# Kernel tuning notes

Measured on AMD Instinct MI355X. Metric: run time of the kernel, lower is better.

## Reference

```python
import jax, jax.numpy as jnp
import numpy as np

D_MODEL, N_HEADS, HEAD_DIM, D_STATE, CHUNK, N_GROUPS = 3584, 112, 64, 64, 256, 2


def setup_inputs() -> dict:
    key = jax.random.key(0)
    ks = jax.random.split(key, 8)
    b, l = 1, 4096
    inner = N_HEADS * HEAD_DIM
    scale = 0.02  # keep activations well-scaled (nn.Linear-ish init)
    return {
        "hidden_states": jax.random.normal(ks[0], (b, l, D_MODEL), jnp.float32),
        "W_in": jax.random.normal(ks[1], (2 * inner, D_MODEL), jnp.float32) * scale,
        "W_out": jax.random.normal(ks[2], (D_MODEL, inner), jnp.float32) * scale,
        "A_log": jax.random.normal(ks[3], (N_HEADS,), jnp.float32),
        "D": jnp.ones((N_HEADS,), jnp.float32),
        "dt_bias": jax.random.normal(ks[4], (N_HEADS,), jnp.float32),
        "B": jax.random.normal(ks[5], (b, l, N_GROUPS, D_STATE), jnp.float32),
        "C": jax.random.normal(ks[6], (b, l, N_GROUPS, D_STATE), jnp.float32),
    }


def _segsum(x):
    # x: [..., T] -> [..., T, T]; segsum[i,j] = sum_{j<k<=i} x[k], -inf above diag
    T = x.shape[-1]
    cs = jnp.cumsum(x, axis=-1)
    diff = cs[..., :, None] - cs[..., None, :]
    mask = jnp.tril(jnp.ones((T, T), bool))
    return jnp.where(mask, diff, -jnp.inf)


def reference(hidden_states, W_in, W_out, A_log, D, dt_bias, B, C):
    b, l, _ = hidden_states.shape
    h, p, n, c = N_HEADS, HEAD_DIM, D_STATE, CHUNK
    nc = l // c

    xz = hidden_states @ W_in.T                       # [b,l,2*h*p]
    x, z = jnp.split(xz, 2, axis=-1)
    x = x.reshape(b, l, h, p)

    dt = jnp.full((b, l, h), 0.1, hidden_states.dtype)  # module uses constant 0.1
    A = -jnp.exp(A_log)                                  # [h]
    dt_sp = jax.nn.softplus(dt + dt_bias)                # [b,l,h]

    # expand group-shared B/C to per-head
    Bh = jnp.repeat(B, h // N_GROUPS, axis=2)            # [b,l,h,n]
    Ch = jnp.repeat(C, h // N_GROUPS, axis=2)

    xdt = x * dt_sp[..., None]                           # discretized input dt*x

    # chunked views: k = chunk index, i/j = position within chunk
    xc = xdt.reshape(b, nc, c, h, p)
    Bc = Bh.reshape(b, nc, c, h, n)
    Cc = Ch.reshape(b, nc, c, h, n)
    dA = (dt_sp * A).reshape(b, nc, c, h).transpose(0, 3, 1, 2)  # [b,h,nc,c]
    dA_cs = jnp.cumsum(dA, axis=-1)                               # [b,h,nc,c]

    # 1) intra-chunk (diagonal blocks)
    L = jnp.exp(_segsum(dA))                                      # [b,h,nc,c,c]
    Y_diag = jnp.einsum('bkihn,bkjhn,bhkij,bkjhp->bkihp', Cc, Bc, L, xc)

    # 2) per-chunk end states
    decay_states = jnp.exp(dA_cs[..., -1:] - dA_cs)               # [b,h,nc,c]
    states = jnp.einsum('bkjhn,bhkj,bkjhp->bkhpn', Bc, decay_states, xc)

    # 3) inter-chunk recurrence: S_k = exp(sum dA_k) * S_{k-1} + states_k
    chunk_decay = jnp.exp(dA_cs[..., -1])                         # [b,h,nc]

    def step(carry, inp):
        dec, st = inp                      # dec: [b,h], st: [b,h,p,n]
        new = carry * dec[..., None, None] + st
        return new, carry                  # emit state ENTERING this chunk

    _, prev = jax.lax.scan(
        step,
        jnp.zeros_like(states[:, 0]),
        (chunk_decay.transpose(2, 0, 1), states.transpose(1, 0, 2, 3, 4)),
    )
    prev = prev.transpose(1, 0, 2, 3, 4)                          # [b,nc,h,p,n]

    # 4) inter-chunk output contribution
    Y_off = jnp.einsum('bkihn,bkhpn,bhki->bkihp', Cc, prev, jnp.exp(dA_cs))

    y = (Y_diag + Y_off).reshape(b, l, h, p) + x * D[None, None, :, None]
    y = y.reshape(b, l, h * p) * jax.nn.sigmoid(z)                # gated
    return y @ W_out.T
```

## Files before the change

kernel.cpp:

```cpp
#include <hip/hip_runtime.h>
#include <hip/hip_bf16.h>

typedef __bf16 bf16;
typedef bf16 bf16x4 __attribute__((ext_vector_type(4)));
typedef bf16 bf16x8 __attribute__((ext_vector_type(8)));
typedef float f32x4 __attribute__((ext_vector_type(4)));

#define GLDS(g, l)                                                            \
  __builtin_amdgcn_global_load_lds(                                           \
      (const __attribute__((address_space(1))) void*)(g),                     \
      (__attribute__((address_space(3))) void*)(l), 16, 0, 0)

constexpr int DM = 3584;
constexpr int NH = 112;
constexpr int HD = 64;
constexpr int DSTATE = 64;
constexpr int CH = 256;
constexpr int NG = 2;
constexpr int SEQ = 4096;
constexpr int INNER = NH * HD;
constexpr int NCHUNK = SEQ / CH;
constexpr int HPG = NH / NG;

__device__ __forceinline__ float softplus_f(float x) {
  return x > 15.f ? x : log1pf(expf(x));
}

__device__ __forceinline__ f32x4 mfma_bf16(bf16x8 a, bf16x8 b, f32x4 c) {
  return __builtin_amdgcn_mfma_f32_16x16x32_bf16(a, b, c, 0, 0, 0);
}

__global__ __launch_bounds__(256) void k_cvt(const float* __restrict__ in,
                                             bf16* __restrict__ out, int n4) {
  int i = blockIdx.x * 256 + threadIdx.x;
  if (i >= n4) return;
  float4 v = reinterpret_cast<const float4*>(in)[i];
  bf16x4 o;
  o[0] = (bf16)v.x; o[1] = (bf16)v.y; o[2] = (bf16)v.z; o[3] = (bf16)v.w;
  reinterpret_cast<bf16x4*>(out)[i] = o;
}

template <int MODE>
__global__ __launch_bounds__(256) void k_gemm(const bf16* __restrict__ A,
                                              const bf16* __restrict__ B,
                                              void* __restrict__ outp, int K) {
  __shared__ alignas(16) bf16 As[128 * 32];
  __shared__ alignas(16) bf16 Bs[128 * 32];
  const int t = threadIdx.x;
  const int wave = t >> 6, lane = t & 63;
  const int quad = lane >> 4, l16 = lane & 15;
  const int wm = (wave >> 1) * 64, wn = (wave & 1) * 64;
  const long m0 = (long)blockIdx.y * 128, n0 = (long)blockIdx.x * 128;

  const int r_s = t >> 2, c_s = (t & 3) * 8;
  const bf16* gA = A + (m0 + r_s) * (long)K + c_s;
  const bf16* gB = B + (n0 + r_s) * (long)K + c_s;
  const long rowstep = (long)64 * K;

  f32x4 acc[4][4] = {};

  for (int k0 = 0; k0 < K; k0 += 32) {
    __syncthreads();
    GLDS(gA, &As[t * 8]);
    GLDS(gA + rowstep, &As[(t + 256) * 8]);
    GLDS(gB, &Bs[t * 8]);
    GLDS(gB + rowstep, &Bs[(t + 256) * 8]);
    gA += 32; gB += 32;
    __syncthreads();
    bf16x8 af[4], bfr[4];
#pragma unroll
    for (int i = 0; i < 4; i++)
      af[i] = *reinterpret_cast<const bf16x8*>(&As[(wm + i * 16 + l16) * 32 + quad * 8]);
#pragma unroll
    for (int j = 0; j < 4; j++)
      bfr[j] = *reinterpret_cast<const bf16x8*>(&Bs[(wn + j * 16 + l16) * 32 + quad * 8]);
#pragma unroll
    for (int i = 0; i < 4; i++)
#pragma unroll
      for (int j = 0; j < 4; j++)
        acc[i][j] = mfma_bf16(af[i], bfr[j], acc[i][j]);
  }

#pragma unroll
  for (int i = 0; i < 4; i++)
#pragma unroll
    for (int j = 0; j < 4; j++) {
      long col = n0 + wn + j * 16 + l16;
      long mg = m0 + wm + i * 16 + quad * 4;
      if constexpr (MODE == 0) {
        bf16* o = (bf16*)outp;
        bf16x4 v;
#pragma unroll
        for (int u = 0; u < 4; u++) v[u] = (bf16)acc[i][j][u];
        *reinterpret_cast<bf16x4*>(&o[col * SEQ + mg]) = v;
      } else if constexpr (MODE == 1) {
        bf16* o = (bf16*)outp;
#pragma unroll
        for (int u = 0; u < 4; u++) o[(mg + u) * (long)INNER + col] = (bf16)acc[i][j][u];
      } else {
        float* o = (float*)outp;
#pragma unroll
        for (int u = 0; u < 4; u++) o[(mg + u) * (long)DM + col] = acc[i][j][u];
      }
    }
}

__global__ __launch_bounds__(256) void k_states(const bf16* __restrict__ xT,
                                                const bf16* __restrict__ Bbf,
                                                const float* __restrict__ A_log,
                                                const float* __restrict__ dt_bias,
                                                float* __restrict__ states) {
  const int kc = blockIdx.x;
  const int h = blockIdx.y;
  const int g = h / HPG;
  const int t = threadIdx.x;
  const int wave = t >> 6, lane = t & 63, quad = lane >> 4, l16 = lane & 15;
  const float dts = softplus_f(0.1f + dt_bias[h]);
  const float dAh = -expf(A_log[h]) * dts;

  __shared__ alignas(16) bf16 xTs[64 * 136];
  __shared__ alignas(16) bf16 BTs[64 * 136];

  const bf16* srcX = xT + (size_t)h * 64 * SEQ + (size_t)kc * CH;
  const bf16* srcB = Bbf + ((size_t)kc * CH * NG + g) * DSTATE;

  f32x4 acc[4] = {};

  for (int half = 0; half < 2; half++) {
    __syncthreads();
#pragma unroll
    for (int q = 0; q < 4; q++) {
      int u = q * 256 + t;
      int row = u >> 4, c8 = (u & 15) * 8;
      bf16x8 v = *reinterpret_cast<const bf16x8*>(&srcX[(size_t)row * SEQ + half * 128 + c8]);
      *reinterpret_cast<bf16x8*>(&xTs[row * 136 + c8]) = v;
    }
#pragma unroll
    for (int q = 0; q < 4; q++) {
      int u = q * 256 + t;
      int jl = u & 127, n8 = (u >> 7) * 8;
      int j = half * 128 + jl;
      bf16x8 v = *reinterpret_cast<const bf16x8*>(&srcB[(size_t)j * (NG * DSTATE) + n8]);
      float s = expf(dAh * (float)(CH - 1 - j));
#pragma unroll
      for (int e = 0; e < 8; e++)
        BTs[(n8 + e) * 136 + jl] = (bf16)((float)v[e] * s);
    }
    __syncthreads();
#pragma unroll
    for (int kk = 0; kk < 4; kk++) {
      bf16x8 a = *reinterpret_cast<const bf16x8*>(&xTs[(wave * 16 + l16) * 136 + kk * 32 + quad * 8]);
#pragma unroll
      for (int tn = 0; tn < 4; tn++) {
        bf16x8 b = *reinterpret_cast<const bf16x8*>(&BTs[(tn * 16 + l16) * 136 + kk * 32 + quad * 8]);
        acc[tn] = mfma_bf16(a, b, acc[tn]);
      }
    }
  }
  float* dst = states + (size_t)(kc * NH + h) * 64 * 64;
#pragma unroll
  for (int tn = 0; tn < 4; tn++)
#pragma unroll
    for (int u = 0; u < 4; u++) {
      int p = wave * 16 + quad * 4 + u;
      dst[p * 64 + tn * 16 + l16] = acc[tn][u] * dts;
    }
}

__global__ __launch_bounds__(256) void k_scan(float* __restrict__ states,
                                              const float* __restrict__ A_log,
                                              const float* __restrict__ dt_bias) {
  int idx = blockIdx.x * 256 + threadIdx.x;
  int h = idx >> 12;
  int pn = idx & 4095;
  float dts = softplus_f(0.1f + dt_bias[h]);
  float dAh = -expf(A_log[h]) * dts;
  float cd = expf(dAh * (float)CH);
  float carry = 0.f;
  float* p = states + (size_t)h * 4096 + pn;
  const size_t stride = (size_t)NH * 4096;
#pragma unroll
  for (int k = 0; k < NCHUNK; k++) {
    float s = p[k * stride];
    p[k * stride] = carry;
    carry = carry * cd + s;
  }
}

__global__ __launch_bounds__(256) void k_y(const bf16* __restrict__ xT,
                                           const bf16* __restrict__ Bbf,
                                           const bf16* __restrict__ Cbf,
                                           const float* __restrict__ prev,
                                           bf16* __restrict__ zy,
                                           const float* __restrict__ A_log,
                                           const float* __restrict__ Dvec,
                                           const float* __restrict__ dt_bias) {
  const int half = blockIdx.x;
  const int kc = blockIdx.y;
  const int h = blockIdx.z;
  const int g = h / HPG;
  const int i0 = half * 128;
  const int t = threadIdx.x;
  const int wave = t >> 6, lane = t & 63, quad = lane >> 4, l16 = lane & 15;
  const float dts = softplus_f(0.1f + dt_bias[h]);
  const float dAh = -expf(A_log[h]) * dts;
  const float Dh = Dvec[h];

  __shared__ alignas(16) bf16 Cs[128 * 72];
  __shared__ alignas(16) bf16 Bsh[64 * 72];
  __shared__ alignas(16) bf16 xTs[64 * 72];
  __shared__ alignas(16) bf16 Ws[128 * 72];

  {
    const bf16* src = Cbf + ((size_t)(kc * CH + i0) * NG + g) * DSTATE;
#pragma unroll
    for (int q = 0; q < 4; q++) {
      int u = q * 256 + t;
      int row = u >> 3, c8 = (u & 7) * 8;
      bf16x8 v = *reinterpret_cast<const bf16x8*>(&src[(size_t)row * (NG * DSTATE) + c8]);
      *reinterpret_cast<bf16x8*>(&Cs[row * 72 + c8]) = v;
    }
  }
  {
    const float* src = prev + (size_t)(kc * NH + h) * 4096;
#pragma unroll
    for (int q = 0; q < 4; q++) {
      int u = q * 256 + t;
      int p = u >> 4, c4 = (u & 15) * 4;
      float4 v = *reinterpret_cast<const float4*>(&src[p * 64 + c4]);
      bf16x4 o;
      o[0] = (bf16)v.x; o[1] = (bf16)v.y; o[2] = (bf16)v.z; o[3] = (bf16)v.w;
      *reinterpret_cast<bf16x4*>(&Bsh[p * 72 + c4]) = o;
    }
  }
  __syncthreads();

  f32x4 accY[2][4] = {};
#pragma unroll
  for (int kk = 0; kk < 2; kk++) {
    bf16x8 a0 = *reinterpret_cast<const bf16x8*>(&Cs[(wave * 32 + l16) * 72 + kk * 32 + quad * 8]);
    bf16x8 a1 = *reinterpret_cast<const bf16x8*>(&Cs[(wave * 32 + 16 + l16) * 72 + kk * 32 + quad * 8]);
#pragma unroll
    for (int tn = 0; tn < 4; tn++) {
      bf16x8 b = *reinterpret_cast<const bf16x8*>(&Bsh[(tn * 16 + l16) * 72 + kk * 32 + quad * 8]);
      accY[0][tn] = mfma_bf16(a0, b, accY[0][tn]);
      accY[1][tn] = mfma_bf16(a1, b, accY[1][tn]);
    }
  }
#pragma unroll
  for (int tm = 0; tm < 2; tm++)
#pragma unroll
    for (int u = 0; u < 4; u++) {
      float sc = expf(dAh * (float)(i0 + wave * 32 + tm * 16 + quad * 4 + u + 1));
#pragma unroll
      for (int tn = 0; tn < 4; tn++) accY[tm][tn][u] *= sc;
    }

  const int npan = half ? 4 : 2;
  for (int jb = 0; jb < npan; jb++) {
    __syncthreads();
    {
      const bf16* src = Bbf + ((size_t)(kc * CH + jb * 64) * NG + g) * DSTATE;
#pragma unroll
      for (int q = 0; q < 2; q++) {
        int u = q * 256 + t;
        int row = u >> 3, c8 = (u & 7) * 8;
        bf16x8 v = *reinterpret_cast<const bf16x8*>(&src[(size_t)row * (NG * DSTATE) + c8]);
        *reinterpret_cast<bf16x8*>(&Bsh[row * 72 + c8]) = v;
      }
    }
    {
      const bf16* src = xT + (size_t)h * 64 * SEQ + (size_t)kc * CH + jb * 64;
#pragma unroll
      for (int q = 0; q < 2; q++) {
        int u = q * 256 + t;
        int row = u >> 3, c8 = (u & 7) * 8;
        bf16x8 v = *reinterpret_cast<const bf16x8*>(&src[(size_t)row * SEQ + c8]);
        *reinterpret_cast<bf16x8*>(&xTs[row * 72 + c8]) = v;
      }
    }
    __syncthreads();
    f32x4 accS[2][4] = {};
#pragma unroll
    for (int kk = 0; kk < 2; kk++) {
      bf16x8 a0 = *reinterpret_cast<const bf16x8*>(&Cs[(wave * 32 + l16) * 72 + kk * 32 + quad * 8]);
      bf16x8 a1 = *reinterpret_cast<const bf16x8*>(&Cs[(wave * 32 + 16 + l16) * 72 + kk * 32 + quad * 8]);
#pragma unroll
      for (int tj = 0; tj < 4; tj++) {
        bf16x8 b = *reinterpret_cast<const bf16x8*>(&Bsh[(tj * 16 + l16) * 72 + kk * 32 + quad * 8]);
        accS[0][tj] = mfma_bf16(a0, b, accS[0][tj]);
        accS[1][tj] = mfma_bf16(a1, b, accS[1][tj]);
      }
    }
#pragma unroll
    for (int tm = 0; tm < 2; tm++)
#pragma unroll
      for (int tj = 0; tj < 4; tj++)
#pragma unroll
        for (int u = 0; u < 4; u++) {
          int li = wave * 32 + tm * 16 + quad * 4 + u;
          int ai = i0 + li;
          int aj = jb * 64 + tj * 16 + l16;
          float s = (ai >= aj) ? dts * expf(dAh * (float)(ai - aj)) : 0.f;
          Ws[li * 72 + tj * 16 + l16] = (bf16)(accS[tm][tj][u] * s);
        }
#pragma unroll
    for (int kk = 0; kk < 2; kk++) {
      bf16x8 a0 = *reinterpret_cast<const bf16x8*>(&Ws[(wave * 32 + l16) * 72 + kk * 32 + quad * 8]);
      bf16x8 a1 = *reinterpret_cast<const bf16x8*>(&Ws[(wave * 32 + 16 + l16) * 72 + kk * 32 + quad * 8]);
#pragma unroll
      for (int tn = 0; tn < 4; tn++) {
        bf16x8 b = *reinterpret_cast<const bf16x8*>(&xTs[(tn * 16 + l16) * 72 + kk * 32 + quad * 8]);
        accY[0][tn] = mfma_bf16(a0, b, accY[0][tn]);
        accY[1][tn] = mfma_bf16(a1, b, accY[1][tn]);
      }
    }
  }

#pragma unroll
  for (int tm = 0; tm < 2; tm++)
#pragma unroll
    for (int tn = 0; tn < 4; tn++)
#pragma unroll
      for (int u = 0; u < 4; u++) {
        int li = wave * 32 + tm * 16 + quad * 4 + u;
        long lg = (long)kc * CH + i0 + li;
        int p = tn * 16 + l16;
        float xv = (float)xT[(size_t)(h * 64 + p) * SEQ + lg];
        float yv = accY[tm][tn][u] + xv * Dh;
        size_t off = (size_t)lg * INNER + h * 64 + p;
        float zv = (float)zy[off];
        float gate = 1.f / (1.f + expf(-zv));
        zy[off] = (bf16)(yv * gate);
      }
}

extern "C" void kernel_launch(void* const* d_in, const int* in_sizes, int n_in,
                              void* d_out, int out_size, void* d_ws, size_t ws_size,
                              hipStream_t stream) {
  const float* hs    = (const float*)d_in[0];
  const float* W_in  = (const float*)d_in[1];
  const float* W_out = (const float*)d_in[2];
  const float* A_log = (const float*)d_in[3];
  const float* Dv    = (const float*)d_in[4];
  const float* dtb   = (const float*)d_in[5];
  const float* Bin   = (const float*)d_in[6];
  const float* Cin   = (const float*)d_in[7];

  char* ws = (char*)d_ws;
  size_t off = 0;
  auto alloc = [&](size_t bytes) {
    void* p = ws + off;
    off += (bytes + 255) & ~(size_t)255;
    return p;
  };
  bf16* wbuf = (bf16*)alloc((size_t)INNER * DM * 2);
  bf16* hsb  = (bf16*)alloc((size_t)SEQ * DM * 2);
  bf16* xTg  = (bf16*)alloc((size_t)INNER * SEQ * 2);
  bf16* zy   = (bf16*)alloc((size_t)SEQ * INNER * 2);
  bf16* Bbf  = (bf16*)alloc((size_t)SEQ * NG * DSTATE * 2);
  bf16* Cbf  = (bf16*)alloc((size_t)SEQ * NG * DSTATE * 2);
  float* st  = (float*)alloc((size_t)NCHUNK * NH * 64 * 64 * 4);

  auto cvt = [&](const float* src, bf16* dst, size_t n) {
    int n4 = (int)(n / 4);
    k_cvt<<<dim3((n4 + 255) / 256), dim3(256), 0, stream>>>(src, dst, n4);
  };

  cvt(hs, hsb, (size_t)SEQ * DM);
  cvt(Bin, Bbf, (size_t)SEQ * NG * DSTATE);
  cvt(Cin, Cbf, (size_t)SEQ * NG * DSTATE);

  dim3 blk(256);
  dim3 g1(INNER / 128, SEQ / 128);

  cvt(W_in, wbuf, (size_t)INNER * DM);
  k_gemm<0><<<g1, blk, 0, stream>>>(hsb, wbuf, xTg, DM);
  cvt(W_in + (size_t)INNER * DM, wbuf, (size_t)INNER * DM);
  k_gemm<1><<<g1, blk, 0, stream>>>(hsb, wbuf, zy, DM);
  cvt(W_out, wbuf, (size_t)DM * INNER);

  k_states<<<dim3(NCHUNK, NH), blk, 0, stream>>>(xTg, Bbf, A_log, dtb, st);
  k_scan<<<dim3((NH * 4096) / 256), blk, 0, stream>>>(st, A_log, dtb);
  k_y<<<dim3(2, NCHUNK, NH), blk, 0, stream>>>(xTg, Bbf, Cbf, st, zy, A_log, Dv, dtb);

  dim3 g2(DM / 128, SEQ / 128);
  k_gemm<2><<<g2, blk, 0, stream>>>(zy, wbuf, d_out, INNER);

  (void)in_sizes; (void)n_in; (void)out_size; (void)ws_size;
}
```

Baseline: 1.438 ms.

## Rewrite GEMM with 256x256 tiles, 8 waves, pipelined LDS prefetch and swizzle

Replaces the 128x128 single-buffered bf16 GEMM with a 256x256 tile kernel using 512 threads, double-buffered LDS staging via global_load_lds, XOR-swizzled LDS layout, interleaved load/MFMA phases with explicit vmcnt waits and setprio, and grid swizzling for L2 locality. The aim is to raise arithmetic intensity and hide global-load latency in the three large projection GEMMs. In exchange it uses 128KB LDS per block and many accumulator registers, which limits occupancy. The tight hand-written synchronisation also makes the kernel more fragile.

```diff
diff --git a/kernel.cpp b/kernel.cpp
--- a/kernel.cpp
+++ b/kernel.cpp
@@ -30,6 +30,12 @@
   return __builtin_amdgcn_mfma_f32_16x16x32_bf16(a, b, c, 0, 0, 0);
 }
 
+__device__ __forceinline__ void wgbar() {
+  asm volatile("" ::: "memory");
+  __builtin_amdgcn_s_barrier();
+  asm volatile("" ::: "memory");
+}
+
 __global__ __launch_bounds__(256) void k_cvt(const float* __restrict__ in,
                                              bf16* __restrict__ out, int n4) {
   int i = blockIdx.x * 256 + threadIdx.x;
@@ -41,66 +47,137 @@
 }
 
 template <int MODE>
-__global__ __launch_bounds__(256) void k_gemm(const bf16* __restrict__ A,
-                                              const bf16* __restrict__ B,
-                                              void* __restrict__ outp, int K) {
-  __shared__ alignas(16) bf16 As[128 * 32];
-  __shared__ alignas(16) bf16 Bs[128 * 32];
+__global__ __launch_bounds__(512, 2) void k_gemm(const bf16* __restrict__ A,
+                                                 const bf16* __restrict__ B,
+                                                 void* __restrict__ outp, int K) {
+  __shared__ alignas(16) bf16 lds[65536];
+  char* ldsb = (char*)lds;
+
   const int t = threadIdx.x;
-  const int wave = t >> 6, lane = t & 63;
-  const int quad = lane >> 4, l16 = lane & 15;
-  const int wm = (wave >> 1) * 64, wn = (wave & 1) * 64;
-  const long m0 = (long)blockIdx.y * 128, n0 = (long)blockIdx.x * 128;
-
-  const int r_s = t >> 2, c_s = (t & 3) * 8;
-  const bf16* gA = A + (m0 + r_s) * (long)K + c_s;
-  const bf16* gB = B + (n0 + r_s) * (long)K + c_s;
-  const long rowstep = (long)64 * K;
-
-  f32x4 acc[4][4] = {};
-
-  for (int k0 = 0; k0 < K; k0 += 32) {
-    __syncthreads();
-    GLDS(gA, &As[t * 8]);
-    GLDS(gA + rowstep, &As[(t + 256) * 8]);
-    GLDS(gB, &Bs[t * 8]);
-    GLDS(gB + rowstep, &Bs[(t + 256) * 8]);
-    gA += 32; gB += 32;
-    __syncthreads();
-    bf16x8 af[4], bfr[4];
-#pragma unroll
-    for (int i = 0; i < 4; i++)
-      af[i] = *reinterpret_cast<const bf16x8*>(&As[(wm + i * 16 + l16) * 32 + quad * 8]);
-#pragma unroll
-    for (int j = 0; j < 4; j++)
-      bfr[j] = *reinterpret_cast<const bf16x8*>(&Bs[(wn + j * 16 + l16) * 32 + quad * 8]);
-#pragma unroll
-    for (int i = 0; i < 4; i++)
-#pragma unroll
-      for (int j = 0; j < 4; j++)
-        acc[i][j] = mfma_bf16(af[i], bfr[j], acc[i][j]);
-  }
-
-#pragma unroll
-  for (int i = 0; i < 4; i++)
-#pragma unroll
-    for (int j = 0; j < 4; j++) {
-      long col = n0 + wn + j * 16 + l16;
-      long mg = m0 + wm + i * 16 + quad * 4;
+  const int lane = t & 63, wv = t >> 6;
+  const int wm = wv >> 2, wn = wv & 3;
+  const int l16 = lane & 15, quad = lane >> 4;
+
+  int nwg = gridDim.x * gridDim.y;
+  int orig = blockIdx.y * gridDim.x + blockIdx.x;
+  int swz = (nwg & 7) ? orig : (orig & 7) * (nwg >> 3) + (orig >> 3);
+  const long n0 = (long)(swz % gridDim.x) * 256;
+  const long m0 = (long)(swz / gridDim.x) * 256;
+
+  const int r2 = t >> 3;
+  const int cgl = (t & 7) ^ (r2 & 7);
+  const int gsr = r2 * 2 + (cgl >> 2);
+  const int cel = (cgl & 3) * 8;
+  const bf16* pA0 = A + (m0 + gsr) * (size_t)K + cel;
+  const bf16* pA1 = pA0 + (size_t)128 * K;
+  const bf16* pB0 = B + (n0 + gsr) * (size_t)K + cel;
+  const bf16* pB1 = pB0 + (size_t)128 * K;
+
+  const int swzr = (((l16 & 1) << 2) + quad) ^ ((l16 >> 1) & 7);
+  const int offA = (wm * 64 + (l16 >> 1)) * 128 + swzr * 16;
+  const int offB = (wn * 32 + (l16 >> 1)) * 128 + swzr * 16;
+
+  f32x4 acc[8][4] = {};
+  bf16x8 af[4], bfr[4];
+  const int NT = K >> 6;
+
+#define STG_A(koff, slot)                        \
+  GLDS(pA0 + (koff), ldsb + (slot) + t * 16);    \
+  GLDS(pA1 + (koff), ldsb + (slot) + 8192 + t * 16)
+#define STG_B(koff, slot)                        \
+  GLDS(pB0 + (koff), ldsb + (slot) + t * 16);    \
+  GLDS(pB1 + (koff), ldsb + (slot) + 8192 + t * 16)
+#define LD_A(mh, slot)                                                 \
+  _Pragma("unroll") for (int mf = 0; mf < 4; ++mf)                     \
+      af[mf] = *reinterpret_cast<const bf16x8*>(                       \
+          ldsb + (slot) + offA + ((mh) * 4 + mf) * 1024)
+#define LD_B(slot)                                                     \
+  _Pragma("unroll") for (int nf = 0; nf < 4; ++nf)                     \
+      bfr[nf] = *reinterpret_cast<const bf16x8*>(                      \
+          ldsb + (slot) + offB + nf * 1024)
+#define MFMA16(mh)                                                     \
+  __builtin_amdgcn_s_setprio(1);                                       \
+  _Pragma("unroll") for (int mf = 0; mf < 4; ++mf)                     \
+      _Pragma("unroll") for (int nf = 0; nf < 4; ++nf)                 \
+          acc[(mh) * 4 + mf][nf] =                                     \
+              mfma_bf16(af[mf], bfr[nf], acc[(mh) * 4 + mf][nf]);      \
+  __builtin_amdgcn_s_setprio(0)
+#define VMW(n) asm volatile("s_waitcnt vmcnt(" #n ")" ::: "memory")
+
+  STG_A(0, 0);
+  STG_B(0, 65536);
+  STG_A(32, 16384);
+  STG_B(32, 65536 + 16384);
+  STG_A(64, 32768);
+  STG_B(64, 65536 + 32768);
+  VMW(8);
+  wgbar();
+
+  int buf = 0;
+  for (int tt = 0; tt < NT; ++tt, buf ^= 1) {
+    const int aB = buf * 32768, oB = 32768 - aB;
+    const int sA0 = aB, sA1 = aB + 16384;
+    const int sB0 = 65536 + aB, sB1 = 65536 + aB + 16384;
+    const int oA1 = oB + 16384, oB1 = 65536 + oB + 16384;
+    const int k1 = (tt + 1) * 64 + 32;
+    const int k2 = (tt + 2) * 64;
+
+    LD_B(sB0);
+    LD_A(0, sA0);
+    if (tt + 1 < NT) { STG_A(k1, oA1); }
+    wgbar();
+    MFMA16(0);
+    wgbar();
+    LD_A(1, sA0);
+    if (tt + 1 < NT) { STG_B(k1, oB1); }
+    wgbar();
+    MFMA16(1);
+    if (tt + 1 < NT) { VMW(8); } else { VMW(0); }
+    wgbar();
+    LD_B(sB1);
+    LD_A(0, sA1);
+    if (tt + 2 < NT) { STG_A(k2, sA0); }
+    wgbar();
+    MFMA16(0);
+    wgbar();
+    LD_A(1, sA1);
+    if (tt + 2 < NT) { STG_B(k2, sB0); }
+    wgbar();
+    MFMA16(1);
+    if (tt + 2 < NT) { VMW(8); }
+    else if (tt + 1 < NT) { VMW(4); }
+    wgbar();
+  }
+
+#undef STG_A
+#undef STG_B
+#undef LD_A
+#undef LD_B
+#undef MFMA16
+#undef VMW
+
+#pragma unroll
+  for (int mf = 0; mf < 8; ++mf)
+#pragma unroll
+    for (int nf = 0; nf < 4; ++nf) {
+      long col = n0 + wn * 64 + nf * 16 + l16;
+      long mg = m0 + wm * 128 + mf * 16 + quad * 4;
       if constexpr (MODE == 0) {
         bf16* o = (bf16*)outp;
         bf16x4 v;
 #pragma unroll
-        for (int u = 0; u < 4; u++) v[u] = (bf16)acc[i][j][u];
+        for (int u = 0; u < 4; u++) v[u] = (bf16)acc[mf][nf][u];
         *reinterpret_cast<bf16x4*>(&o[col * SEQ + mg]) = v;
       } else if constexpr (MODE == 1) {
         bf16* o = (bf16*)outp;
 #pragma unroll
-        for (int u = 0; u < 4; u++) o[(mg + u) * (long)INNER + col] = (bf16)acc[i][j][u];
+        for (int u = 0; u < 4; u++)
+          o[(mg + u) * (long)INNER + col] = (bf16)acc[mf][nf][u];
       } else {
         float* o = (float*)outp;
 #pragma unroll
-        for (int u = 0; u < 4; u++) o[(mg + u) * (long)DM + col] = acc[i][j][u];
+        for (int u = 0; u < 4; u++)
+          o[(mg + u) * (long)DM + col] = acc[mf][nf][u];
       }
     }
 }
@@ -372,20 +449,21 @@
   cvt(Cin, Cbf, (size_t)SEQ * NG * DSTATE);
 
   dim3 blk(256);
-  dim3 g1(INNER / 128, SEQ / 128);
+  dim3 gblk(512);
+  dim3 g1(INNER / 256, SEQ / 256);
+  dim3 g2(DM / 256, SEQ / 256);
 
   cvt(W_in, wbuf, (size_t)INNER * DM);
-  k_gemm<0><<<g1, blk, 0, stream>>>(hsb, wbuf, xTg, DM);
+  k_gemm<0><<<g1, gblk, 0, stream>>>(hsb, wbuf, xTg, DM);
   cvt(W_in + (size_t)INNER * DM, wbuf, (size_t)INNER * DM);
-  k_gemm<1><<<g1, blk, 0, stream>>>(hsb, wbuf, zy, DM);
+  k_gemm<1><<<g1, gblk, 0, stream>>>(hsb, wbuf, zy, DM);
   cvt(W_out, wbuf, (size_t)DM * INNER);
 
   k_states<<<dim3(NCHUNK, NH), blk, 0, stream>>>(xTg, Bbf, A_log, dtb, st);
   k_scan<<<dim3((NH * 4096) / 256), blk, 0, stream>>>(st, A_log, dtb);
   k_y<<<dim3(2, NCHUNK, NH), blk, 0, stream>>>(xTg, Bbf, Cbf, st, zy, A_log, Dv, dtb);
 
-  dim3 g2(DM / 128, SEQ / 128);
-  k_gemm<2><<<g2, blk, 0, stream>>>(zy, wbuf, d_out, INNER);
+  k_gemm<2><<<g2, gblk, 0, stream>>>(zy, wbuf, d_out, INNER);
 
   (void)in_sizes; (void)n_in; (void)out_size; (void)ws_size;
 }
```

Result: faster. 1.174 ms (-18.3%).
